# Kernel optimization log

Measured on AMD Instinct MI355X. Metric: run time of the kernel, lower is better.

## Reference

```python
import jax, jax.numpy as jnp
import numpy as np

NEG_INF = -1e9


def setup_inputs() -> dict:
    key = jax.random.key(0)
    k1, k2, k3 = jax.random.split(key, 3)
    B, N, F_IN, F_OUT = 8, 4096, 128, 64
    h = jax.random.normal(k1, (B, N, F_IN), dtype=jnp.float32)
    # xavier_uniform with gain=1.414 on [F_IN, F_OUT]
    limit = 1.414 * np.sqrt(6.0 / (F_IN + F_OUT))
    W = jax.random.uniform(k2, (F_IN, F_OUT), dtype=jnp.float32, minval=-limit, maxval=limit)
    adj = jax.random.randint(k3, (N, N), 0, 2, dtype=jnp.int32)
    return {"h": h, "W": W, "adj": adj}


def reference(h, W, adj):
    # h: [B, N, F_in], W: [F_in, F_out], adj: [N, N]
    F_out = W.shape[1]
    Wh = jnp.einsum('bnf,fo->bno', h, W)                      # [B, N, F_out]
    scores = jnp.einsum('bnd,bmd->bnm', Wh, Wh) / np.sqrt(F_out).astype(np.float32)
    attention = jnp.where(adj[None, :, :] > 0, scores, NEG_INF)
    attention = jax.nn.softmax(attention, axis=2)             # [B, N, N]
    # dropout p=0.0 / eval mode -> identity
    h_prime = jnp.einsum('bnm,bmd->bnd', attention, Wh)       # [B, N, F_out]
    return jax.nn.elu(h_prime)  # concat=True path
```

## Files before the change

### kernel.cpp

```cpp
#include <hip/hip_runtime.h>

typedef _Float16 half8  __attribute__((ext_vector_type(8)));
typedef float    float4v __attribute__((ext_vector_type(4)));

#define N_ 4096
#define B_ 8
#define D_ 64
#define F_ 128

__global__ __launch_bounds__(256) void pack_adj_kernel(const int4* __restrict__ adj4,
                                                       unsigned long long* __restrict__ bits) {
  __shared__ unsigned char nib[256];
  const int t = threadIdx.x;
  int4 v = adj4[(size_t)blockIdx.x * 256 + t];
  unsigned n = (v.x > 0 ? 1u : 0u) | (v.y > 0 ? 2u : 0u) |
               (v.z > 0 ? 4u : 0u) | (v.w > 0 ? 8u : 0u);
  nib[t] = (unsigned char)n;
  __syncthreads();
  if (t < 16) {
    const unsigned char* p = &nib[t * 16];
    unsigned long long wv = 0;
#pragma unroll
    for (int i = 0; i < 16; ++i) wv |= (unsigned long long)p[i] << (4 * i);
    bits[(size_t)blockIdx.x * 16 + t] = wv;
  }
}

__global__ __launch_bounds__(256) void wh_kernel(const float* __restrict__ h,
                                                 const float* __restrict__ W,
                                                 _Float16* __restrict__ Wh16,
                                                 _Float16* __restrict__ WhT16) {
  __shared__ __align__(16) _Float16 hs[64 * 128];
  __shared__ __align__(16) _Float16 wt[64 * 128];
  __shared__ __align__(16) _Float16 otile[64][72];
  const int t = threadIdx.x;
  const int rowbase = blockIdx.x * 64;
#pragma unroll
  for (int i = 0; i < 4; ++i) {
    int e = i * 256 + t;
    int r = e >> 4, kb = e & 15;
    const float4v* src = (const float4v*)(h + (size_t)(rowbase + r) * F_ + kb * 8);
    float4v a = src[0], b = src[1];
    uint4 pk;
    pk.x = __builtin_bit_cast(unsigned, __builtin_amdgcn_cvt_pkrtz(a[0], a[1]));
    pk.y = __builtin_bit_cast(unsigned, __builtin_amdgcn_cvt_pkrtz(a[2], a[3]));
    pk.z = __builtin_bit_cast(unsigned, __builtin_amdgcn_cvt_pkrtz(b[0], b[1]));
    pk.w = __builtin_bit_cast(unsigned, __builtin_amdgcn_cvt_pkrtz(b[2], b[3]));
    *(uint4*)&hs[(r * 16 + (kb ^ (r & 7))) * 8] = pk;
  }
#pragma unroll
  for (int k = 0; k < 8; ++k) {
    int i4 = t + k * 256;
    float4v v = ((const float4v*)W)[i4];
    int f = i4 >> 4, c4 = (i4 & 15) * 4;
    int oct = f >> 3, ki = f & 7;
#pragma unroll
    for (int j = 0; j < 4; ++j) {
      int c = c4 + j;
      wt[(c * 16 + (oct ^ (c & 7))) * 8 + ki] = (_Float16)v[j];
    }
  }
  __syncthreads();
  const int w = t >> 6, lane = t & 63;
  const int g = lane >> 4, c = lane & 15;
  const int r0 = w * 16;
  const int arow = r0 + c, aswz = arow & 7;
  half8 af[4];
#pragma unroll
  for (int kk = 0; kk < 4; ++kk)
    af[kk] = *(half8*)&hs[(arow * 16 + ((kk * 4 + g) ^ aswz)) * 8];
  float4v acc[4];
#pragma unroll
  for (int cb = 0; cb < 4; ++cb) {
    float4v z = (float4v){0.f, 0.f, 0.f, 0.f};
    const int bcol = cb * 16 + c, bswz = c & 7;
#pragma unroll
    for (int kk = 0; kk < 4; ++kk) {
      half8 bf = *(half8*)&wt[(bcol * 16 + ((kk * 4 + g) ^ bswz)) * 8];
      z = __builtin_amdgcn_mfma_f32_16x16x32_f16(af[kk], bf, z, 0, 0, 0);
    }
    acc[cb] = z;
  }
  __syncthreads();
#pragma unroll
  for (int cb = 0; cb < 4; ++cb)
#pragma unroll
    for (int j = 0; j < 4; ++j)
      otile[r0 + g * 4 + j][cb * 16 + c] = (_Float16)acc[cb][j];
  __syncthreads();
  const int rr = t >> 2, c0 = (t & 3) * 16;
  half8 w0 = *(half8*)&otile[rr][c0];
  half8 w1 = *(half8*)&otile[rr][c0 + 8];
  _Float16* dW = Wh16 + (size_t)(rowbase + rr) * D_ + c0;
  *(half8*)dW       = w0;
  *(half8*)(dW + 8) = w1;
  const int dl = t >> 2, k0t = (t & 3) * 16;
  half8 o0, o1;
#pragma unroll
  for (int i = 0; i < 8; ++i) o0[i] = otile[k0t + i][dl];
#pragma unroll
  for (int i = 0; i < 8; ++i) o1[i] = otile[k0t + 8 + i][dl];
  const int b = rowbase >> 12, n0 = rowbase & 4095;
  _Float16* dst = WhT16 + ((size_t)(b * D_ + dl)) * N_ + n0 + k0t;
  *(half8*)dst       = o0;
  *(half8*)(dst + 8) = o1;
}

__global__ __launch_bounds__(512, 4) void attn_kernel(
    const unsigned long long* __restrict__ bits,
    const _Float16* __restrict__ Wh,
    const _Float16* __restrict__ WhT,
    float* __restrict__ out) {
  __shared__ __align__(16) char lds[81920];
  const int tid  = threadIdx.x;
  const int w    = tid >> 6;
  const int lane = tid & 63;
  const int g    = lane >> 4;
  const int c    = lane & 15;
  const int qi   = w & 3;
  const int s    = w >> 2;
  const int bid  = blockIdx.x;
  const int b    = bid >> 6;
  const int q0b  = (bid & 63) * 64;
  const int q0w  = q0b + qi * 16;

  const _Float16* Whb  = Wh  + (size_t)b * N_ * D_;
  const _Float16* WhTb = WhT + (size_t)b * D_ * N_;
  char* Kbase = lds + s * 16384;
  char* Vbase = lds + 32768 + s * 16384;
  char* Pb    = lds + 65536 + w * 2048;

  const int e0  = (qi * 2 + 0) * 64 + lane;
  const int e1  = (qi * 2 + 1) * 64 + lane;
  const int r0e = e0 >> 3, s0e = (e0 & 7) ^ (r0e & 7);
  const int r1e = e1 >> 3, s1e = (e1 & 7) ^ (r1e & 7);

  half8 qf[2];
#pragma unroll
  for (int ds = 0; ds < 2; ++ds) {
    half8 v = *(const half8*)(Whb + (size_t)(q0w + c) * D_ + ds * 32 + g * 8);
    qf[ds] = v * (_Float16)0.18033688f;
  }

  float4v o_acc[4];
#pragma unroll
  for (int d = 0; d < 4; ++d) o_acc[d] = (float4v){0.f, 0.f, 0.f, 0.f};
  float mrow = -1e30f, lrow = 0.f;

  const unsigned long long* bq = bits + (size_t)(q0w + c) * 64 + s * 32;

  const _Float16* pk0 = Whb + (size_t)(s * 2048 + r0e) * D_ + s0e * 8;
  const _Float16* pk1 = Whb + (size_t)(s * 2048 + r1e) * D_ + s1e * 8;
  const _Float16* pv0 = WhTb + (size_t)r0e * N_ + s * 2048 + s0e * 8;
  const _Float16* pv1 = WhTb + (size_t)r1e * N_ + s * 2048 + s1e * 8;

  *(half8*)(Kbase + e0 * 16) = *(const half8*)pk0;
  *(half8*)(Kbase + e1 * 16) = *(const half8*)pk1;
  *(half8*)(Vbase + e0 * 16) = *(const half8*)pv0;
  *(half8*)(Vbase + e1 * 16) = *(const half8*)pv1;
  unsigned long long bw = bq[0];
  __syncthreads();

#define COMPUTE_TILE(CUR)                                                          \
  {                                                                                \
    const _Float16* Kc = (const _Float16*)(Kbase + (CUR));                         \
    const _Float16* Vc = (const _Float16*)(Vbase + (CUR));                         \
    float4v sac[4];                                                                \
    _Pragma("unroll")                                                              \
    for (int st = 0; st < 4; ++st) {                                               \
      const _Float16* kr = Kc + (st * 16 + c) * 64;                                \
      half8 kf0 = *(const half8*)(kr + ((g       ^ (c & 7)) * 8));                 \
      half8 kf1 = *(const half8*)(kr + (((g + 4) ^ (c & 7)) * 8));                 \
      float4v z = (float4v){0.f, 0.f, 0.f, 0.f};                                   \
      z = __builtin_amdgcn_mfma_f32_16x16x32_f16(kf0, qf[0], z, 0, 0, 0);          \
      z = __builtin_amdgcn_mfma_f32_16x16x32_f16(kf1, qf[1], z, 0, 0, 0);          \
      sac[st] = z;                                                                 \
    }                                                                              \
    _Pragma("unroll")                                                              \
    for (int st = 0; st < 4; ++st) {                                               \
      unsigned wb = (unsigned)(bw >> (st * 16 + g * 4));                           \
      _Pragma("unroll")                                                            \
      for (int j = 0; j < 4; ++j)                                                  \
        sac[st][j] = (wb & (1u << j)) ? sac[st][j] : -1e9f;                        \
    }                                                                              \
    float ta = fmaxf(fmaxf(sac[0][0], sac[0][1]), fmaxf(sac[0][2], sac[0][3]));    \
    float tb = fmaxf(fmaxf(sac[1][0], sac[1][1]), fmaxf(sac[1][2], sac[1][3]));    \
    float tc = fmaxf(fmaxf(sac[2][0], sac[2][1]), fmaxf(sac[2][2], sac[2][3]));    \
    float td = fmaxf(fmaxf(sac[3][0], sac[3][1]), fmaxf(sac[3][2], sac[3][3]));    \
    float tmax = fmaxf(fmaxf(ta, tb), fmaxf(tc, td));                              \
    tmax = fmaxf(tmax, __shfl_xor(tmax, 16));                                      \
    tmax = fmaxf(tmax, __shfl_xor(tmax, 32));                                      \
    if (__any(tmax > mrow)) {                                                      \
      float mnew  = fmaxf(mrow, tmax);                                             \
      float alpha = exp2f(mrow - mnew);                                            \
      mrow = mnew;                                                                 \
      lrow *= alpha;                                                               \
      _Pragma("unroll")                                                            \
      for (int j = 0; j < 4; ++j) {                                                \
        float aj = __shfl(alpha, (lane & 48) | (g * 4 + j));                       \
        _Pragma("unroll")                                                          \
        for (int d = 0; d < 4; ++d) o_acc[d][j] *= aj;                             \
      }                                                                            \
    }                                                                              \
    _Pragma("unroll")                                                              \
    for (int st = 0; st < 4; ++st) {                                               \
      float p0 = exp2f(sac[st][0] - mrow);                                         \
      float p1 = exp2f(sac[st][1] - mrow);                                         \
      float p2 = exp2f(sac[st][2] - mrow);                                         \
      float p3 = exp2f(sac[st][3] - mrow);                                         \
      lrow += (p0 + p1) + (p2 + p3);                                               \
      uint2 pr;                                                                    \
      pr.x = __builtin_bit_cast(unsigned, __builtin_amdgcn_cvt_pkrtz(p0, p1));     \
      pr.y = __builtin_bit_cast(unsigned, __builtin_amdgcn_cvt_pkrtz(p2, p3));     \
      const int cell = st * 2 + (g >> 1);                                          \
      *(uint2*)(Pb + (cell * 16 + c) * 16 + (g & 1) * 8) = pr;                     \
    }                                                                              \
    _Pragma("unroll")                                                              \
    for (int ks = 0; ks < 2; ++ks) {                                               \
      half8 afp = *(const half8*)(Pb + ((ks * 4 + g) * 16 + c) * 16);              \
      _Pragma("unroll")                                                            \
      for (int d = 0; d < 4; ++d) {                                                \
        half8 vf = *(const half8*)(Vc + (d * 16 + c) * 64 +                        \
                                   (((ks * 4 + g) ^ (c & 7)) * 8));                \
        o_acc[d] = __builtin_amdgcn_mfma_f32_16x16x32_f16(afp, vf, o_acc[d],       \
                                                          0, 0, 0);                \
      }                                                                            \
    }                                                                              \
  }

  int cur = 0;
#pragma unroll 2
  for (int t = 0; t < 31; ++t) {
    pk0 += 64 * D_; pk1 += 64 * D_; pv0 += 64; pv1 += 64;
    half8 ka = *(const half8*)pk0;
    half8 kb = *(const half8*)pk1;
    half8 va = *(const half8*)pv0;
    half8 vb = *(const half8*)pv1;
    unsigned long long bwn = bq[t + 1];

    COMPUTE_TILE(cur)

    const int nxt = cur ^ 8192;
    *(half8*)(Kbase + nxt + e0 * 16) = ka;
    *(half8*)(Kbase + nxt + e1 * 16) = kb;
    *(half8*)(Vbase + nxt + e0 * 16) = va;
    *(half8*)(Vbase + nxt + e1 * 16) = vb;
    __syncthreads();
    cur = nxt;
    bw = bwn;
  }
  COMPUTE_TILE(cur)
#undef COMPUTE_TILE

  lrow += __shfl_xor(lrow, 16);
  lrow += __shfl_xor(lrow, 32);
  __syncthreads();
  float* Ob = (float*)lds;
#pragma unroll
  for (int d = 0; d < 4; ++d)
#pragma unroll
    for (int j = 0; j < 4; ++j)
      Ob[(w * 16 + g * 4 + j) * 66 + d * 16 + c] = o_acc[d][j];
  float2* mlb = (float2*)(lds + 36864);
  if (g == 0) mlb[w * 16 + c] = make_float2(mrow, lrow);
  __syncthreads();

#pragma unroll
  for (int it = 0; it < 8; ++it) {
    int r   = w + it * 8;
    int col = lane;
    int qq = r >> 4, rl = r & 15;
    float2 ml0 = mlb[qq * 16 + rl];
    float2 ml1 = mlb[(qq + 4) * 16 + rl];
    float mm = fmaxf(ml0.x, ml1.x);
    float a0 = exp2f(ml0.x - mm);
    float a1 = exp2f(ml1.x - mm);
    float l  = a0 * ml0.y + a1 * ml1.y;
    float o  = a0 * Ob[(qq * 16 + rl) * 66 + col] + a1 * Ob[((qq + 4) * 16 + rl) * 66 + col];
    float x  = o / l;
    x = x > 0.f ? x : (__expf(x) - 1.f);
    out[((size_t)b * N_ + q0b + r) * D_ + col] = x;
  }
}

extern "C" void kernel_launch(void* const* d_in, const int* in_sizes, int n_in,
                              void* d_out, int out_size, void* d_ws, size_t ws_size,
                              hipStream_t stream) {
  const float* h = (const float*)d_in[0];
  const float* W = (const float*)d_in[1];
  const int* adj = (const int*)d_in[2];
  float* out = (float*)d_out;

  char* ws = (char*)d_ws;
  unsigned long long* bits = (unsigned long long*)ws;
  _Float16* Wh16  = (_Float16*)(ws + (2u << 20));
  _Float16* WhT16 = (_Float16*)(ws + (6u << 20));

  hipLaunchKernelGGL(pack_adj_kernel, dim3((N_ * N_) / 1024), dim3(256), 0, stream,
                     (const int4*)adj, bits);
  hipLaunchKernelGGL(wh_kernel,   dim3((B_ * N_) / 64), dim3(256), 0, stream, h, W, Wh16, WhT16);
  hipLaunchKernelGGL(attn_kernel, dim3(B_ * (N_ / 64)), dim3(512), 0, stream, bits, Wh16, WhT16, out);
}
```

Before: 191.9 us.

## Split attention keys four ways across 1024-thread blocks with smaller tiles

The attention kernel now runs 16 waves per block instead of 8, splitting each block's key range into four groups of 1024 keys rather than two of 2048. Each group streams 32-key K/V tiles through double-buffered LDS, using a new swizzle for the transposed V tile. s_setprio is raised around the MFMA sections, and the epilogue merges four partial softmax states per row instead of two. The aim is more in-flight waves and more latency hiding per CU. In exchange, the register budget per thread is tighter, barriers are more frequent with less work per tile, and the final merge costs more.

```diff
diff --git a/kernel.cpp b/kernel.cpp
--- a/kernel.cpp
+++ b/kernel.cpp
@@ -1,6 +1,7 @@
 #include <hip/hip_runtime.h>
 
 typedef _Float16 half8  __attribute__((ext_vector_type(8)));
+typedef _Float16 half4v __attribute__((ext_vector_type(4)));
 typedef float    float4v __attribute__((ext_vector_type(4)));
 
 #define N_ 4096
@@ -106,7 +107,7 @@
   *(half8*)(dst + 8) = o1;
 }
 
-__global__ __launch_bounds__(512, 4) void attn_kernel(
+__global__ __launch_bounds__(1024, 8) void attn_kernel(
     const unsigned long long* __restrict__ bits,
     const _Float16* __restrict__ Wh,
     const _Float16* __restrict__ WhT,
@@ -126,14 +127,13 @@
 
   const _Float16* Whb  = Wh  + (size_t)b * N_ * D_;
   const _Float16* WhTb = WhT + (size_t)b * D_ * N_;
-  char* Kbase = lds + s * 16384;
-  char* Vbase = lds + 32768 + s * 16384;
-  char* Pb    = lds + 65536 + w * 2048;
-
-  const int e0  = (qi * 2 + 0) * 64 + lane;
-  const int e1  = (qi * 2 + 1) * 64 + lane;
-  const int r0e = e0 >> 3, s0e = (e0 & 7) ^ (r0e & 7);
-  const int r1e = e1 >> 3, s1e = (e1 & 7) ^ (r1e & 7);
+  char* Kgrp = lds + s * 16384;
+  char* Pb   = lds + 65536 + w * 1024;
+
+  const int li  = qi * 64 + lane;
+  const int rK  = li >> 3, oK = (li & 7) ^ (rK & 7);
+  const int rV  = li >> 2, oV = (li & 3) ^ ((rV ^ (rV >> 2)) & 3);
+  const int vswz = (c ^ (c >> 2)) & 3;
 
   half8 qf[2];
 #pragma unroll
@@ -147,104 +147,95 @@
   for (int d = 0; d < 4; ++d) o_acc[d] = (float4v){0.f, 0.f, 0.f, 0.f};
   float mrow = -1e30f, lrow = 0.f;
 
-  const unsigned long long* bq = bits + (size_t)(q0w + c) * 64 + s * 32;
-
-  const _Float16* pk0 = Whb + (size_t)(s * 2048 + r0e) * D_ + s0e * 8;
-  const _Float16* pk1 = Whb + (size_t)(s * 2048 + r1e) * D_ + s1e * 8;
-  const _Float16* pv0 = WhTb + (size_t)r0e * N_ + s * 2048 + s0e * 8;
-  const _Float16* pv1 = WhTb + (size_t)r1e * N_ + s * 2048 + s1e * 8;
-
-  *(half8*)(Kbase + e0 * 16) = *(const half8*)pk0;
-  *(half8*)(Kbase + e1 * 16) = *(const half8*)pk1;
-  *(half8*)(Vbase + e0 * 16) = *(const half8*)pv0;
-  *(half8*)(Vbase + e1 * 16) = *(const half8*)pv1;
-  unsigned long long bw = bq[0];
-  __syncthreads();
-
-#define COMPUTE_TILE(CUR)                                                          \
-  {                                                                                \
-    const _Float16* Kc = (const _Float16*)(Kbase + (CUR));                         \
-    const _Float16* Vc = (const _Float16*)(Vbase + (CUR));                         \
-    float4v sac[4];                                                                \
-    _Pragma("unroll")                                                              \
-    for (int st = 0; st < 4; ++st) {                                               \
-      const _Float16* kr = Kc + (st * 16 + c) * 64;                                \
-      half8 kf0 = *(const half8*)(kr + ((g       ^ (c & 7)) * 8));                 \
-      half8 kf1 = *(const half8*)(kr + (((g + 4) ^ (c & 7)) * 8));                 \
-      float4v z = (float4v){0.f, 0.f, 0.f, 0.f};                                   \
-      z = __builtin_amdgcn_mfma_f32_16x16x32_f16(kf0, qf[0], z, 0, 0, 0);          \
-      z = __builtin_amdgcn_mfma_f32_16x16x32_f16(kf1, qf[1], z, 0, 0, 0);          \
-      sac[st] = z;                                                                 \
-    }                                                                              \
-    _Pragma("unroll")                                                              \
-    for (int st = 0; st < 4; ++st) {                                               \
-      unsigned wb = (unsigned)(bw >> (st * 16 + g * 4));                           \
-      _Pragma("unroll")                                                            \
-      for (int j = 0; j < 4; ++j)                                                  \
-        sac[st][j] = (wb & (1u << j)) ? sac[st][j] : -1e9f;                        \
-    }                                                                              \
-    float ta = fmaxf(fmaxf(sac[0][0], sac[0][1]), fmaxf(sac[0][2], sac[0][3]));    \
-    float tb = fmaxf(fmaxf(sac[1][0], sac[1][1]), fmaxf(sac[1][2], sac[1][3]));    \
-    float tc = fmaxf(fmaxf(sac[2][0], sac[2][1]), fmaxf(sac[2][2], sac[2][3]));    \
-    float td = fmaxf(fmaxf(sac[3][0], sac[3][1]), fmaxf(sac[3][2], sac[3][3]));    \
-    float tmax = fmaxf(fmaxf(ta, tb), fmaxf(tc, td));                              \
-    tmax = fmaxf(tmax, __shfl_xor(tmax, 16));                                      \
-    tmax = fmaxf(tmax, __shfl_xor(tmax, 32));                                      \
-    if (__any(tmax > mrow)) {                                                      \
-      float mnew  = fmaxf(mrow, tmax);                                             \
-      float alpha = exp2f(mrow - mnew);                                            \
-      mrow = mnew;                                                                 \
-      lrow *= alpha;                                                               \
-      _Pragma("unroll")                                                            \
-      for (int j = 0; j < 4; ++j) {                                                \
-        float aj = __shfl(alpha, (lane & 48) | (g * 4 + j));                       \
-        _Pragma("unroll")                                                          \
-        for (int d = 0; d < 4; ++d) o_acc[d][j] *= aj;                             \
-      }                                                                            \
-    }                                                                              \
-    _Pragma("unroll")                                                              \
-    for (int st = 0; st < 4; ++st) {                                               \
-      float p0 = exp2f(sac[st][0] - mrow);                                         \
-      float p1 = exp2f(sac[st][1] - mrow);                                         \
-      float p2 = exp2f(sac[st][2] - mrow);                                         \
-      float p3 = exp2f(sac[st][3] - mrow);                                         \
-      lrow += (p0 + p1) + (p2 + p3);                                               \
-      uint2 pr;                                                                    \
-      pr.x = __builtin_bit_cast(unsigned, __builtin_amdgcn_cvt_pkrtz(p0, p1));     \
-      pr.y = __builtin_bit_cast(unsigned, __builtin_amdgcn_cvt_pkrtz(p2, p3));     \
-      const int cell = st * 2 + (g >> 1);                                          \
-      *(uint2*)(Pb + (cell * 16 + c) * 16 + (g & 1) * 8) = pr;                     \
-    }                                                                              \
-    _Pragma("unroll")                                                              \
-    for (int ks = 0; ks < 2; ++ks) {                                               \
-      half8 afp = *(const half8*)(Pb + ((ks * 4 + g) * 16 + c) * 16);              \
-      _Pragma("unroll")                                                            \
-      for (int d = 0; d < 4; ++d) {                                                \
-        half8 vf = *(const half8*)(Vc + (d * 16 + c) * 64 +                        \
-                                   (((ks * 4 + g) ^ (c & 7)) * 8));                \
-        o_acc[d] = __builtin_amdgcn_mfma_f32_16x16x32_f16(afp, vf, o_acc[d],       \
-                                                          0, 0, 0);                \
-      }                                                                            \
-    }                                                                              \
+  const unsigned* bqp = (const unsigned*)bits + (size_t)(q0w + c) * 128 + s * 32;
+
+  const _Float16* pk = Whb + (size_t)(s * 1024 + rK) * D_ + oK * 8;
+  const _Float16* pv = WhTb + (size_t)rV * N_ + s * 1024 + oV * 8;
+
+  *(half8*)(Kgrp + li * 16)        = *(const half8*)pk;
+  *(half8*)(Kgrp + 4096 + li * 16) = *(const half8*)pv;
+  unsigned bw = bqp[0];
+  __syncthreads();
+
+#define COMPUTE_TILE(CUR)                                                        \
+  {                                                                              \
+    const _Float16* Kc = (const _Float16*)(Kgrp + (CUR));                        \
+    const _Float16* Vc = (const _Float16*)(Kgrp + 4096 + (CUR));                 \
+    float4v sac[2];                                                              \
+    __builtin_amdgcn_s_setprio(1);                                               \
+    _Pragma("unroll")                                                            \
+    for (int st = 0; st < 2; ++st) {                                             \
+      const _Float16* kr = Kc + (st * 16 + c) * 64;                              \
+      half8 kf0 = *(const half8*)(kr + ((g       ^ (c & 7)) * 8));               \
+      half8 kf1 = *(const half8*)(kr + (((g + 4) ^ (c & 7)) * 8));               \
+      float4v z = (float4v){0.f, 0.f, 0.f, 0.f};                                 \
+      z = __builtin_amdgcn_mfma_f32_16x16x32_f16(kf0, qf[0], z, 0, 0, 0);        \
+      z = __builtin_amdgcn_mfma_f32_16x16x32_f16(kf1, qf[1], z, 0, 0, 0);        \
+      sac[st] = z;                                                               \
+    }                                                                            \
+    __builtin_amdgcn_s_setprio(0);                                               \
+    _Pragma("unroll")                                                            \
+    for (int st = 0; st < 2; ++st) {                                             \
+      unsigned wb = bw >> (st * 16 + g * 4);                                     \
+      _Pragma("unroll")                                                          \
+      for (int j = 0; j < 4; ++j)                                                \
+        sac[st][j] = (wb & (1u << j)) ? sac[st][j] : -1e9f;                      \
+    }                                                                            \
+    float tmax = fmaxf(                                                          \
+        fmaxf(fmaxf(sac[0][0], sac[0][1]), fmaxf(sac[0][2], sac[0][3])),         \
+        fmaxf(fmaxf(sac[1][0], sac[1][1]), fmaxf(sac[1][2], sac[1][3])));        \
+    tmax = fmaxf(tmax, __shfl_xor(tmax, 16));                                    \
+    tmax = fmaxf(tmax, __shfl_xor(tmax, 32));                                    \
+    if (__any(tmax > mrow)) {                                                    \
+      float mnew  = fmaxf(mrow, tmax);                                           \
+      float alpha = exp2f(mrow - mnew);                                          \
+      mrow = mnew;                                                               \
+      lrow *= alpha;                                                             \
+      _Pragma("unroll")                                                          \
+      for (int j = 0; j < 4; ++j) {                                              \
+        float aj = __shfl(alpha, (lane & 48) | (g * 4 + j));                     \
+        _Pragma("unroll")                                                        \
+        for (int d = 0; d < 4; ++d) o_acc[d][j] *= aj;                           \
+      }                                                                          \
+    }                                                                            \
+    _Pragma("unroll")                                                            \
+    for (int st = 0; st < 2; ++st) {                                             \
+      float p0 = exp2f(sac[st][0] - mrow);                                       \
+      float p1 = exp2f(sac[st][1] - mrow);                                       \
+      float p2 = exp2f(sac[st][2] - mrow);                                       \
+      float p3 = exp2f(sac[st][3] - mrow);                                       \
+      lrow += (p0 + p1) + (p2 + p3);                                             \
+      uint2 pr;                                                                  \
+      pr.x = __builtin_bit_cast(unsigned, __builtin_amdgcn_cvt_pkrtz(p0, p1));   \
+      pr.y = __builtin_bit_cast(unsigned, __builtin_amdgcn_cvt_pkrtz(p2, p3));   \
+      const int cell = st * 2 + (g >> 1);                                        \
+      *(uint2*)(Pb + (cell * 16 + c) * 16 + (g & 1) * 8) = pr;                   \
+    }                                                                            \
+    half8 afp = *(const half8*)(Pb + (g * 16 + c) * 16);                         \
+    __builtin_amdgcn_s_setprio(1);                                               \
+    _Pragma("unroll")                                                            \
+    for (int d = 0; d < 4; ++d) {                                                \
+      half8 vf = *(const half8*)(Vc + ((d * 16 + c) * 4 + (g ^ vswz)) * 8);      \
+      o_acc[d] = __builtin_amdgcn_mfma_f32_16x16x32_f16(afp, vf, o_acc[d],       \
+                                                        0, 0, 0);                \
+    }                                                                            \
+    __builtin_amdgcn_s_setprio(0);                                               \
   }
 
   int cur = 0;
 #pragma unroll 2
   for (int t = 0; t < 31; ++t) {
-    pk0 += 64 * D_; pk1 += 64 * D_; pv0 += 64; pv1 += 64;
-    half8 ka = *(const half8*)pk0;
-    half8 kb = *(const half8*)pk1;
-    half8 va = *(const half8*)pv0;
-    half8 vb = *(const half8*)pv1;
-    unsigned long long bwn = bq[t + 1];
+    pk += 32 * D_;
+    pv += 32;
+    half8 ka = *(const half8*)pk;
+    half8 va = *(const half8*)pv;
+    unsigned bwn = bqp[t + 1];
 
     COMPUTE_TILE(cur)
 
     const int nxt = cur ^ 8192;
-    *(half8*)(Kbase + nxt + e0 * 16) = ka;
-    *(half8*)(Kbase + nxt + e1 * 16) = kb;
-    *(half8*)(Vbase + nxt + e0 * 16) = va;
-    *(half8*)(Vbase + nxt + e1 * 16) = vb;
+    *(half8*)(Kgrp + nxt + li * 16)        = ka;
+    *(half8*)(Kgrp + nxt + 4096 + li * 16) = va;
     __syncthreads();
     cur = nxt;
     bw = bwn;
@@ -261,23 +252,30 @@
 #pragma unroll
     for (int j = 0; j < 4; ++j)
       Ob[(w * 16 + g * 4 + j) * 66 + d * 16 + c] = o_acc[d][j];
-  float2* mlb = (float2*)(lds + 36864);
+  float2* mlb = (float2*)(lds + 67584);
   if (g == 0) mlb[w * 16 + c] = make_float2(mrow, lrow);
   __syncthreads();
 
 #pragma unroll
-  for (int it = 0; it < 8; ++it) {
-    int r   = w + it * 8;
-    int col = lane;
+  for (int it = 0; it < 4; ++it) {
+    int idx = tid + it * 1024;
+    int r = idx >> 6, col = idx & 63;
     int qq = r >> 4, rl = r & 15;
-    float2 ml0 = mlb[qq * 16 + rl];
-    float2 ml1 = mlb[(qq + 4) * 16 + rl];
-    float mm = fmaxf(ml0.x, ml1.x);
-    float a0 = exp2f(ml0.x - mm);
-    float a1 = exp2f(ml1.x - mm);
-    float l  = a0 * ml0.y + a1 * ml1.y;
-    float o  = a0 * Ob[(qq * 16 + rl) * 66 + col] + a1 * Ob[((qq + 4) * 16 + rl) * 66 + col];
-    float x  = o / l;
+    float2 ml[4];
+    float mm = -1e30f;
+#pragma unroll
+    for (int p = 0; p < 4; ++p) {
+      ml[p] = mlb[(p * 4 + qq) * 16 + rl];
+      mm = fmaxf(mm, ml[p].x);
+    }
+    float l = 0.f, o = 0.f;
+#pragma unroll
+    for (int p = 0; p < 4; ++p) {
+      float a = exp2f(ml[p].x - mm);
+      l += a * ml[p].y;
+      o += a * Ob[((p * 4 + qq) * 16 + rl) * 66 + col];
+    }
+    float x = o / l;
     x = x > 0.f ? x : (__expf(x) - 1.f);
     out[((size_t)b * N_ + q0b + r) * D_ + col] = x;
   }
@@ -299,5 +297,5 @@
   hipLaunchKernelGGL(pack_adj_kernel, dim3((N_ * N_) / 1024), dim3(256), 0, stream,
                      (const int4*)adj, bits);
   hipLaunchKernelGGL(wh_kernel,   dim3((B_ * N_) / 64), dim3(256), 0, stream, h, W, Wh16, WhT16);
-  hipLaunchKernelGGL(attn_kernel, dim3(B_ * (N_ / 64)), dim3(512), 0, stream, bits, Wh16, WhT16, out);
+  hipLaunchKernelGGL(attn_kernel, dim3(B_ * (N_ / 64)), dim3(1024), 0, stream, bits, Wh16, WhT16, out);
 }
```

Result: slower. 254.7 us (+32.8%).
